# Kernel tuning notes

Measured on AMD Instinct MI355X. Metric: run time of the kernel, lower is better.

Reference implementation:

```python
import jax, jax.numpy as jnp
import numpy as np

B, T, D, H = 256, 512, 512, 512


def setup_inputs() -> dict:
    key = jax.random.key(0)
    k1, k2, k3, k4 = jax.random.split(key, 4)
    inputs = jax.random.normal(k1, (B, T, D), dtype=jnp.float32)
    lengths = jax.random.randint(k2, (B,), 0, T).astype(jnp.int32)
    # LSTM params. Flax nn.LSTMCell uses per-gate dense layers:
    #  input dense (with bias) and recurrent dense (no bias). Packing the
    #  four gates (i, f, g, o) into one matrix is mathematically identical.
    Wx = jax.random.normal(k3, (D, 4 * H), dtype=jnp.float32) * (1.0 / np.sqrt(D))
    Wh = jax.random.normal(k4, (H, 4 * H), dtype=jnp.float32) * (1.0 / np.sqrt(H))
    b = jnp.zeros((4 * H,), dtype=jnp.float32)
    return {"inputs": inputs, "lengths": lengths, "Wx": Wx, "Wh": Wh, "b": b}


def reference(inputs, lengths, Wx, Wh, b):
    batch = inputs.shape[0]
    hidden = Wh.shape[0]
    x_tbd = jnp.swapaxes(inputs, 0, 1)  # [T, B, D]

    def step(carry, x_t):
        c, h = carry
        # fused gate pre-activations: [B, 4H]
        z = x_t @ Wx + h @ Wh + b
        i, f, g, o = jnp.split(z, 4, axis=-1)
        i = jax.nn.sigmoid(i)
        f = jax.nn.sigmoid(f)
        g = jnp.tanh(g)
        o = jax.nn.sigmoid(o)
        c_new = f * c + i * g
        h_new = o * jnp.tanh(c_new)
        return (c_new, h_new), h_new

    c0 = jnp.zeros((batch, hidden), dtype=inputs.dtype)
    h0 = jnp.zeros((batch, hidden), dtype=inputs.dtype)
    _, hs = jax.lax.scan(step, (c0, h0), x_tbd)  # hs: [T, B, H]

    # select output at last valid timestep per example
    idx = jnp.maximum(0, lengths - 1)  # [B]
    return hs[idx, jnp.arange(batch), :]  # [B, H]
```

## Files before the change

### kernel.cpp

```cpp
#include <hip/hip_runtime.h>

#define Bb 256
#define Tt 512
#define Dd 512
#define Hh 512
#define KTOT 1024
#define FOURH 2048

typedef __attribute__((ext_vector_type(8))) short bf16x8;
typedef __attribute__((ext_vector_type(4))) float f32x4;

__device__ __forceinline__ unsigned short f2bf(float f) {
    union { float f; unsigned u; } x; x.f = f;
    unsigned u = x.u;
    unsigned r = u + 0x7FFFu + ((u >> 16) & 1u);
    return (unsigned short)(r >> 16);
}
__device__ __forceinline__ float bf2f(unsigned short s) {
    union { unsigned u; float f; } x; x.u = ((unsigned)s) << 16;
    return x.f;
}

__device__ __forceinline__ uint4 load16_sc01(const void* p) {
    uint4 v;
    asm volatile("global_load_dwordx4 %0, %1, off sc0 sc1" : "=v"(v) : "v"(p));
    return v;
}

__global__ void prep_w(const float* __restrict__ Wx, const float* __restrict__ Wh,
                       unsigned short* __restrict__ WT_hi, unsigned short* __restrict__ WT_lo) {
    __shared__ float tile[32][33];
    int n0 = (blockIdx.x & 63) * 32;
    int k0 = (blockIdx.x >> 6) * 32;
    int tx = threadIdx.x & 31;
    int ty = threadIdx.x >> 5;
    for (int q = 0; q < 4; ++q) {
        int k = k0 + ty + q * 8;
        int n = n0 + tx;
        float v = (k < Dd) ? Wx[(size_t)k * FOURH + n] : Wh[(size_t)(k - Dd) * FOURH + n];
        tile[ty + q * 8][tx] = v;
    }
    __syncthreads();
    for (int q = 0; q < 4; ++q) {
        int nl = ty + q * 8;
        int kl = tx;
        float v = tile[kl][nl];
        unsigned short hi = f2bf(v);
        unsigned short lo = f2bf(v - bf2f(hi));
        size_t o = (size_t)(n0 + nl) * KTOT + (size_t)(k0 + kl);
        WT_hi[o] = hi;
        WT_lo[o] = lo;
    }
}

__global__ void init_state3(char* __restrict__ ws, int persist) {
    long i = (long)blockIdx.x * blockDim.x + threadIdx.x;
    if (i < 98304) {
        *(uint4*)(ws + (8u << 20) + i * 16) = (uint4){0, 0, 0, 0};
    }
    if (persist && i < 512) {
        ((unsigned int*)(ws + (8u << 20) + (1536u << 10)))[i] = 0u;
    }
}

__global__ __launch_bounds__(512) void lstm_persist9(
    const float* __restrict__ X, const int* __restrict__ lengths,
    const unsigned short* __restrict__ WT_hi, const unsigned short* __restrict__ WT_lo,
    const float* __restrict__ bias,
    unsigned int* __restrict__ h_pack,
    unsigned int* __restrict__ ctrl,
    float* __restrict__ out)
{
    __shared__ unsigned short HLDS[32768];
    __shared__ unsigned short XLDS[32768];
    __shared__ float zbuf[8][32][17];

    const int bx = blockIdx.x;
    const int group = bx & 7;
    const int slot = bx >> 3;
    const int rt = slot & 7;
    const int cs = slot >> 3;
    const int r0 = rt * 32;
    const int j0h = group * 64 + cs * 16;
    const int tid = threadIdx.x;
    const int w8 = tid >> 6;
    const int lane = tid & 63;
    const int l15 = lane & 15;
    const int q4 = lane >> 4;
    const int klo = q4 * 8;
    const int gate = w8 & 3;
    const int khalf = w8 >> 2;

    const size_t HB = (size_t)Bb * Hh;

    const int colg = gate * 512 + j0h + l15;
    const size_t bbase = (size_t)colg * KTOT + (size_t)khalf * 512;
    const unsigned short* bhp = &WT_hi[bbase];
    const unsigned short* blp = &WT_lo[bbase];

    const int xr = tid >> 4;
    const int xk0 = (tid & 15) * 32;
    const float* xbase = &X[((size_t)(r0 + xr) * Tt) * Dd + xk0];

    const int er = tid >> 4;
    const int ej = tid & 15;
    const int row_g = r0 + er;
    const int col_h = j0h + ej;
    const size_t oidx = (size_t)row_g * Hh + col_h;
    int oT = lengths[row_g] - 1; if (oT < 0) oT = 0;
    const float b0 = bias[col_h], b1 = bias[512 + col_h],
                b2 = bias[1024 + col_h], b3 = bias[1536 + col_h];
    float creg = 0.f;

    unsigned int* myflag = &ctrl[rt * 32];

    for (int t = 0; t < Tt; ++t) {
        const int p_r = t & 1;
        const unsigned int* hp_r = h_pack + (size_t)p_r * HB;
        unsigned int* hp_w = h_pack + (size_t)(p_r ^ 1) * HB;

        uint4 hb[8];
#pragma unroll
        for (int it = 0; it < 4; ++it) {
            const int c = it * 512 + tid;
            const int row = c >> 6, k8 = c & 63;
            const unsigned int* p = hp_r + ((size_t)(r0 + row) * Hh + k8 * 8);
            hb[it * 2] = load16_sc01(p);
            hb[it * 2 + 1] = load16_sc01(p + 4);
        }

        {
            const float* xp = xbase + (size_t)t * Dd;
            float4 xv[8];
#pragma unroll
            for (int i = 0; i < 8; ++i) xv[i] = ((const float4*)xp)[i];
            const int ksx = tid & 15;
            const int mi = xr >> 4, lr = xr & 15;
#pragma unroll
            for (int c2 = 0; c2 < 4; ++c2) {
                float vv[8];
                *(float4*)&vv[0] = xv[2 * c2];
                *(float4*)&vv[4] = xv[2 * c2 + 1];
                bf16x8 hv8, lv8;
#pragma unroll
                for (int e = 0; e < 8; ++e) {
                    unsigned short hs = f2bf(vv[e]);
                    hv8[e] = (short)hs;
                    lv8[e] = (short)f2bf(vv[e] - bf2f(hs));
                }
                const int lnw = (c2 * 16 + lr) ^ (ksx & 7);
                *(bf16x8*)&XLDS[(((0 * 2 + mi) * 16 + ksx) * 64 + lnw) * 8] = hv8;
                *(bf16x8*)&XLDS[(((1 * 2 + mi) * 16 + ksx) * 64 + lnw) * 8] = lv8;
            }
        }

        asm volatile("s_waitcnt vmcnt(0)" ::: "memory");
        __builtin_amdgcn_sched_barrier(0);

#pragma unroll
        for (int it = 0; it < 4; ++it) {
            const int c = it * 512 + tid;
            const int row = c >> 6, k8 = c & 63;
            const int ksh = k8 >> 2, qq = k8 & 3;
            const int mi = row >> 4, lr = row & 15;
            const unsigned int u0 = hb[it * 2].x, u1 = hb[it * 2].y;
            const unsigned int u2 = hb[it * 2].z, u3 = hb[it * 2].w;
            const unsigned int u4 = hb[it * 2 + 1].x, u5 = hb[it * 2 + 1].y;
            const unsigned int u6 = hb[it * 2 + 1].z, u7 = hb[it * 2 + 1].w;
            uint4 hiw, low;
            hiw.x = (u0 >> 16) | (u1 & 0xffff0000u);
            hiw.y = (u2 >> 16) | (u3 & 0xffff0000u);
            hiw.z = (u4 >> 16) | (u5 & 0xffff0000u);
            hiw.w = (u6 >> 16) | (u7 & 0xffff0000u);
            low.x = (u0 & 0xffffu) | (u1 << 16);
            low.y = (u2 & 0xffffu) | (u3 << 16);
            low.z = (u4 & 0xffffu) | (u5 << 16);
            low.w = (u6 & 0xffffu) | (u7 << 16);
            const int lnw = (qq * 16 + lr) ^ (ksh & 7);
            *(uint4*)&HLDS[(((0 * 2 + mi) * 16 + ksh) * 64 + lnw) * 8] = hiw;
            *(uint4*)&HLDS[(((1 * 2 + mi) * 16 + ksh) * 64 + lnw) * 8] = low;
        }
        __syncthreads();

        const unsigned short* ALDS = khalf ? HLDS : XLDS;
        f32x4 acc[2][3];
#pragma unroll
        for (int mi = 0; mi < 2; ++mi)
#pragma unroll
            for (int s = 0; s < 3; ++s)
                acc[mi][s] = (f32x4){0.f, 0.f, 0.f, 0.f};

#pragma unroll
        for (int ks = 0; ks < 16; ++ks) {
            const int kk = ks * 32 + klo;
            const bf16x8 bh = *(const bf16x8*)&bhp[kk];
            const bf16x8 bl = *(const bf16x8*)&blp[kk];
            const int lnr = lane ^ (ks & 7);
#pragma unroll
            for (int mi = 0; mi < 2; ++mi) {
                const bf16x8 ah = *(const bf16x8*)&ALDS[(((0 * 2 + mi) * 16 + ks) * 64 + lnr) * 8];
                const bf16x8 al = *(const bf16x8*)&ALDS[(((1 * 2 + mi) * 16 + ks) * 64 + lnr) * 8];
                acc[mi][0] = __builtin_amdgcn_mfma_f32_16x16x32_bf16(ah, bh, acc[mi][0], 0, 0, 0);
                acc[mi][1] = __builtin_amdgcn_mfma_f32_16x16x32_bf16(ah, bl, acc[mi][1], 0, 0, 0);
                acc[mi][2] = __builtin_amdgcn_mfma_f32_16x16x32_bf16(al, bh, acc[mi][2], 0, 0, 0);
            }
        }

#pragma unroll
        for (int mi = 0; mi < 2; ++mi) {
            const f32x4 z = acc[mi][0] + acc[mi][1] + acc[mi][2];
#pragma unroll
            for (int r = 0; r < 4; ++r)
                zbuf[w8][mi * 16 + q4 * 4 + r][l15] = z[r];
        }
        __syncthreads();

        float zi = zbuf[0][er][ej] + zbuf[4][er][ej] + b0;
        float zf = zbuf[1][er][ej] + zbuf[5][er][ej] + b1;
        float zg = zbuf[2][er][ej] + zbuf[6][er][ej] + b2;
        float zo = zbuf[3][er][ej] + zbuf[7][er][ej] + b3;
        float ig = 1.f / (1.f + expf(-zi));
        float fg = 1.f / (1.f + expf(-zf));
        float gg = tanhf(zg);
        float og = 1.f / (1.f + expf(-zo));
        float cn = fg * creg + ig * gg;
        creg = cn;
        float hn = og * tanhf(cn);
        unsigned short hh = f2bf(hn);
        unsigned short hl = f2bf(hn - bf2f(hh));
        unsigned int up = ((unsigned int)hh << 16) | (unsigned int)hl;
        __hip_atomic_store(&hp_w[oidx], up, __ATOMIC_RELAXED, __HIP_MEMORY_SCOPE_SYSTEM);
        if (t == oT) out[oidx] = hn;

        if (t < Tt - 1) {
            asm volatile("s_waitcnt vmcnt(0)" ::: "memory");
            __syncthreads();
            if (tid == 0) {
                __hip_atomic_fetch_add(myflag, 1u, __ATOMIC_RELAXED, __HIP_MEMORY_SCOPE_SYSTEM);
                const unsigned int tgt = (unsigned int)(t + 1) * 32u;
                while (__hip_atomic_load(myflag, __ATOMIC_RELAXED, __HIP_MEMORY_SCOPE_SYSTEM) < tgt)
                    __builtin_amdgcn_s_sleep(2);
            }
            __syncthreads();
        }
    }
}

__global__ __launch_bounds__(512) void lstm_step4(
    const float* __restrict__ X, const int* __restrict__ lengths,
    const unsigned short* __restrict__ WT_hi, const unsigned short* __restrict__ WT_lo,
    const float* __restrict__ bias,
    float* __restrict__ c_st,
    const unsigned short* __restrict__ h_r_hi, const unsigned short* __restrict__ h_r_lo,
    unsigned short* __restrict__ h_w_hi, unsigned short* __restrict__ h_w_lo,
    float* __restrict__ out, int t)
{
    __shared__ float zbuf[8][16][17];

    const int bx = blockIdx.x;
    const int xcd = bx & 7;
    const int rem = bx >> 3;
    const int m0 = (rem & 15) * 16;
    const int col_group = xcd * 4 + (rem >> 4);
    const int hc0 = col_group * 16;
    const int tid = threadIdx.x;
    const int w8 = tid >> 6;
    const int lane = tid & 63;
    const int gate = w8 & 3;
    const int khalf = w8 >> 2;

    f32x4 ahh = (f32x4){0,0,0,0}, ahl = (f32x4){0,0,0,0}, alh = (f32x4){0,0,0,0};

    const int colk = gate * 512 + hc0 + (lane & 15);
    const size_t bbase = (size_t)colk * KTOT;
    const int klo = (lane >> 4) * 8;
    const int row = m0 + (lane & 15);

    if (khalf == 0) {
        const float* xrow = &X[((size_t)row * Tt + t) * Dd];
        const unsigned short* bhp = &WT_hi[bbase];
        const unsigned short* blp = &WT_lo[bbase];
#pragma unroll
        for (int ks = 0; ks < 16; ++ks) {
            const int kk = ks * 32 + klo;
            const float4 v0 = *(const float4*)&xrow[kk];
            const float4 v1 = *(const float4*)&xrow[kk + 4];
            float vv[8] = {v0.x, v0.y, v0.z, v0.w, v1.x, v1.y, v1.z, v1.w};
            bf16x8 ah, al;
#pragma unroll
            for (int e = 0; e < 8; ++e) {
                unsigned short hi = f2bf(vv[e]);
                ah[e] = (short)hi;
                al[e] = (short)f2bf(vv[e] - bf2f(hi));
            }
            const bf16x8 bh = *(const bf16x8*)&bhp[kk];
            const bf16x8 bl = *(const bf16x8*)&blp[kk];
            ahh = __builtin_amdgcn_mfma_f32_16x16x32_bf16(ah, bh, ahh, 0, 0, 0);
            ahl = __builtin_amdgcn_mfma_f32_16x16x32_bf16(ah, bl, ahl, 0, 0, 0);
            alh = __builtin_amdgcn_mfma_f32_16x16x32_bf16(al, bh, alh, 0, 0, 0);
        }
    } else {
        const unsigned short* hrh = &h_r_hi[(size_t)row * Hh];
        const unsigned short* hrl = &h_r_lo[(size_t)row * Hh];
        const unsigned short* bhp = &WT_hi[bbase + 512];
        const unsigned short* blp = &WT_lo[bbase + 512];
#pragma unroll
        for (int ks = 0; ks < 16; ++ks) {
            const int kk = ks * 32 + klo;
            const bf16x8 ah = *(const bf16x8*)&hrh[kk];
            const bf16x8 al = *(const bf16x8*)&hrl[kk];
            const bf16x8 bh = *(const bf16x8*)&bhp[kk];
            const bf16x8 bl = *(const bf16x8*)&blp[kk];
            ahh = __builtin_amdgcn_mfma_f32_16x16x32_bf16(ah, bh, ahh, 0, 0, 0);
            ahl = __builtin_amdgcn_mfma_f32_16x16x32_bf16(ah, bl, ahl, 0, 0, 0);
            alh = __builtin_amdgcn_mfma_f32_16x16x32_bf16(al, bh, alh, 0, 0, 0);
        }
    }

    const f32x4 z = ahh + ahl + alh;
#pragma unroll
    for (int r = 0; r < 4; ++r)
        zbuf[w8][(lane >> 4) * 4 + r][lane & 15] = z[r];
    __syncthreads();

    if (tid < 256) {
        const int r = tid >> 4;
        const int j = tid & 15;
        const int row_g = m0 + r;
        const int col_g = hc0 + j;
        float zi = zbuf[0][r][j] + zbuf[4][r][j] + bias[col_g];
        float zf = zbuf[1][r][j] + zbuf[5][r][j] + bias[512 + col_g];
        float zg = zbuf[2][r][j] + zbuf[6][r][j] + bias[1024 + col_g];
        float zo = zbuf[3][r][j] + zbuf[7][r][j] + bias[1536 + col_g];
        float ig = 1.f / (1.f + expf(-zi));
        float fg = 1.f / (1.f + expf(-zf));
        float gg = tanhf(zg);
        float og = 1.f / (1.f + expf(-zo));
        const size_t idx = (size_t)row_g * Hh + col_g;
        float cn = fg * c_st[idx] + ig * gg;
        float hn = og * tanhf(cn);
        c_st[idx] = cn;
        unsigned short hh = f2bf(hn);
        h_w_hi[idx] = hh;
        h_w_lo[idx] = f2bf(hn - bf2f(hh));
        int len = lengths[row_g];
        int oidx = len - 1; if (oidx < 0) oidx = 0;
        if (t == oidx) out[idx] = hn;
    }
}

extern "C" void kernel_launch(void* const* d_in, const int* in_sizes, int n_in,
                              void* d_out, int out_size, void* d_ws, size_t ws_size,
                              hipStream_t stream) {
    const float* X = (const float*)d_in[0];
    const int* lengths = (const int*)d_in[1];
    const float* Wx = (const float*)d_in[2];
    const float* Wh = (const float*)d_in[3];
    const float* bias = (const float*)d_in[4];
    float* out = (float*)d_out;

    char* ws = (char*)d_ws;
    unsigned short* WT_hi = (unsigned short*)ws;
    unsigned short* WT_lo = (unsigned short*)(ws + (4u << 20));
    unsigned int* h_pack = (unsigned int*)(ws + (8u << 20));
    unsigned int* ctrl = (unsigned int*)(ws + (8u << 20) + (1536u << 10));
    float* c_st = (float*)(ws + (8u << 20));
    unsigned short* h_base = (unsigned short*)(ws + (8u << 20) + (512u << 10));
    const size_t HB = (size_t)Bb * Hh;
    unsigned short* h_hi0 = h_base;
    unsigned short* h_lo0 = h_base + HB;
    unsigned short* h_hi1 = h_base + 2 * HB;
    unsigned short* h_lo1 = h_base + 3 * HB;

    const size_t NEED_PERSIST = (8u << 20) + (1536u << 10) + 4096u;
    const int can_persist = (ws_size >= NEED_PERSIST) ? 1 : 0;

    hipLaunchKernelGGL(prep_w, dim3(2048), dim3(256), 0, stream, Wx, Wh, WT_hi, WT_lo);
    hipLaunchKernelGGL(init_state3, dim3(512), dim3(256), 0, stream, ws, can_persist);

    hipError_t err = hipErrorUnknown;
    if (can_persist) {
        void* args[] = { (void*)&X, (void*)&lengths, (void*)&WT_hi, (void*)&WT_lo,
                         (void*)&bias, (void*)&h_pack, (void*)&ctrl, (void*)&out };
        err = hipLaunchCooperativeKernel((const void*)lstm_persist9,
                                         dim3(256), dim3(512), args, 0, stream);
    }
    if (err != hipSuccess) {
        for (int t = 0; t < Tt; ++t) {
            const bool even = (t & 1) == 0;
            hipLaunchKernelGGL(lstm_step4, dim3(512), dim3(512), 0, stream,
                               X, lengths, WT_hi, WT_lo, bias, c_st,
                               even ? h_hi0 : h_hi1, even ? h_lo0 : h_lo1,
                               even ? h_hi1 : h_hi0, even ? h_lo1 : h_lo0,
                               out, t);
        }
    }
}
```

Measured before the change: 7.107 ms.

## Exchange hidden state as int16 fixed-point and retile persistent LSTM blocks

```diff
diff --git a/kernel.cpp b/kernel.cpp
--- a/kernel.cpp
+++ b/kernel.cpp
@@ -25,6 +25,16 @@
     uint4 v;
     asm volatile("global_load_dwordx4 %0, %1, off sc0 sc1" : "=v"(v) : "v"(p));
     return v;
+}
+
+__device__ __forceinline__ void i16_to_bf(int v, unsigned short& bh, unsigned short& bl) {
+    int vh = v >> 8;
+    int vl = v & 255;
+    union { float f; unsigned u; } a, b;
+    a.f = (float)vh * 0.0078125f;
+    b.f = (float)vl * 3.0517578125e-05f;
+    bh = (unsigned short)(a.u >> 16);
+    bl = (unsigned short)(b.u >> 16);
 }
 
 __global__ void prep_w(const float* __restrict__ Wx, const float* __restrict__ Wh,
@@ -63,25 +73,23 @@
     }
 }
 
-__global__ __launch_bounds__(512) void lstm_persist9(
+__global__ __launch_bounds__(512) void lstm_persist10(
     const float* __restrict__ X, const int* __restrict__ lengths,
     const unsigned short* __restrict__ WT_hi, const unsigned short* __restrict__ WT_lo,
     const float* __restrict__ bias,
-    unsigned int* __restrict__ h_pack,
+    short* __restrict__ h_i16,
     unsigned int* __restrict__ ctrl,
     float* __restrict__ out)
 {
-    __shared__ unsigned short HLDS[32768];
-    __shared__ unsigned short XLDS[32768];
-    __shared__ float zbuf[8][32][17];
+    __shared__ unsigned short ALDS[32768];
+    __shared__ float zbuf[8][16][17];
 
     const int bx = blockIdx.x;
-    const int group = bx & 7;
-    const int slot = bx >> 3;
-    const int rt = slot & 7;
-    const int cs = slot >> 3;
-    const int r0 = rt * 32;
-    const int j0h = group * 64 + cs * 16;
+    const int g = bx & 7;
+    const int cb = g * 2 + ((bx >> 3) & 1);
+    const int rt = bx >> 4;
+    const int r0 = rt * 16;
+    const int ch0 = cb * 32;
     const int tid = threadIdx.x;
     const int w8 = tid >> 6;
     const int lane = tid & 63;
@@ -89,55 +97,52 @@
     const int q4 = lane >> 4;
     const int klo = q4 * 8;
     const int gate = w8 & 3;
-    const int khalf = w8 >> 2;
+    const int chalf = w8 >> 2;
 
     const size_t HB = (size_t)Bb * Hh;
 
-    const int colg = gate * 512 + j0h + l15;
-    const size_t bbase = (size_t)colg * KTOT + (size_t)khalf * 512;
+    const int colg = gate * 512 + ch0 + chalf * 16 + l15;
+    const size_t bbase = (size_t)colg * KTOT;
     const unsigned short* bhp = &WT_hi[bbase];
     const unsigned short* blp = &WT_lo[bbase];
 
-    const int xr = tid >> 4;
-    const int xk0 = (tid & 15) * 32;
-    const float* xbase = &X[((size_t)(r0 + xr) * Tt) * Dd + xk0];
-
-    const int er = tid >> 4;
-    const int ej = tid & 15;
+    const int xr = tid >> 5;
+    const int xc = tid & 31;
+    const float* xbase = &X[((size_t)(r0 + xr) * Tt) * Dd + xc * 16];
+
+    const int hr = tid >> 5;
+    const int j = tid & 31;
+
+    const int er = tid >> 5;
+    const int ej = tid & 31;
     const int row_g = r0 + er;
-    const int col_h = j0h + ej;
+    const int col_h = ch0 + ej;
     const size_t oidx = (size_t)row_g * Hh + col_h;
     int oT = lengths[row_g] - 1; if (oT < 0) oT = 0;
     const float b0 = bias[col_h], b1 = bias[512 + col_h],
                 b2 = bias[1024 + col_h], b3 = bias[1536 + col_h];
+    const int ech = ej >> 4;
+    const int ecj = ej & 15;
     float creg = 0.f;
 
     unsigned int* myflag = &ctrl[rt * 32];
 
     for (int t = 0; t < Tt; ++t) {
         const int p_r = t & 1;
-        const unsigned int* hp_r = h_pack + (size_t)p_r * HB;
-        unsigned int* hp_w = h_pack + (size_t)(p_r ^ 1) * HB;
-
-        uint4 hb[8];
-#pragma unroll
-        for (int it = 0; it < 4; ++it) {
-            const int c = it * 512 + tid;
-            const int row = c >> 6, k8 = c & 63;
-            const unsigned int* p = hp_r + ((size_t)(r0 + row) * Hh + k8 * 8);
-            hb[it * 2] = load16_sc01(p);
-            hb[it * 2 + 1] = load16_sc01(p + 4);
-        }
+        const short* hp_r = h_i16 + (size_t)p_r * HB;
+        short* hp_w = h_i16 + (size_t)(p_r ^ 1) * HB;
+
+        const short* hsrc = hp_r + (size_t)(r0 + hr) * Hh + j * 16;
+        uint4 ha = load16_sc01(hsrc);
+        uint4 hb2 = load16_sc01(hsrc + 8);
 
         {
             const float* xp = xbase + (size_t)t * Dd;
-            float4 xv[8];
-#pragma unroll
-            for (int i = 0; i < 8; ++i) xv[i] = ((const float4*)xp)[i];
-            const int ksx = tid & 15;
-            const int mi = xr >> 4, lr = xr & 15;
-#pragma unroll
-            for (int c2 = 0; c2 < 4; ++c2) {
+            float4 xv[4];
+#pragma unroll
+            for (int i = 0; i < 4; ++i) xv[i] = ((const float4*)xp)[i];
+#pragma unroll
+            for (int c2 = 0; c2 < 2; ++c2) {
                 float vv[8];
                 *(float4*)&vv[0] = xv[2 * c2];
                 *(float4*)&vv[4] = xv[2 * c2 + 1];
@@ -148,9 +153,12 @@
                     hv8[e] = (short)hs;
                     lv8[e] = (short)f2bf(vv[e] - bf2f(hs));
                 }
-                const int lnw = (c2 * 16 + lr) ^ (ksx & 7);
-                *(bf16x8*)&XLDS[(((0 * 2 + mi) * 16 + ksx) * 64 + lnw) * 8] = hv8;
-                *(bf16x8*)&XLDS[(((1 * 2 + mi) * 16 + ksx) * 64 + lnw) * 8] = lv8;
+                const int k = xc * 16 + c2 * 8;
+                const int ks = k >> 5;
+                const int qq = (k >> 3) & 3;
+                const int slot = (qq * 16 + xr) ^ (ks & 7);
+                *(bf16x8*)&ALDS[((0 * 32 + ks) * 64 + slot) * 8] = hv8;
+                *(bf16x8*)&ALDS[((1 * 32 + ks) * 64 + slot) * 8] = lv8;
             }
         }
 
@@ -158,67 +166,52 @@
         __builtin_amdgcn_sched_barrier(0);
 
 #pragma unroll
-        for (int it = 0; it < 4; ++it) {
-            const int c = it * 512 + tid;
-            const int row = c >> 6, k8 = c & 63;
-            const int ksh = k8 >> 2, qq = k8 & 3;
-            const int mi = row >> 4, lr = row & 15;
-            const unsigned int u0 = hb[it * 2].x, u1 = hb[it * 2].y;
-            const unsigned int u2 = hb[it * 2].z, u3 = hb[it * 2].w;
-            const unsigned int u4 = hb[it * 2 + 1].x, u5 = hb[it * 2 + 1].y;
-            const unsigned int u6 = hb[it * 2 + 1].z, u7 = hb[it * 2 + 1].w;
-            uint4 hiw, low;
-            hiw.x = (u0 >> 16) | (u1 & 0xffff0000u);
-            hiw.y = (u2 >> 16) | (u3 & 0xffff0000u);
-            hiw.z = (u4 >> 16) | (u5 & 0xffff0000u);
-            hiw.w = (u6 >> 16) | (u7 & 0xffff0000u);
-            low.x = (u0 & 0xffffu) | (u1 << 16);
-            low.y = (u2 & 0xffffu) | (u3 << 16);
-            low.z = (u4 & 0xffffu) | (u5 << 16);
-            low.w = (u6 & 0xffffu) | (u7 << 16);
-            const int lnw = (qq * 16 + lr) ^ (ksh & 7);
-            *(uint4*)&HLDS[(((0 * 2 + mi) * 16 + ksh) * 64 + lnw) * 8] = hiw;
-            *(uint4*)&HLDS[(((1 * 2 + mi) * 16 + ksh) * 64 + lnw) * 8] = low;
+        for (int b = 0; b < 2; ++b) {
+            const uint4 q = b ? hb2 : ha;
+            const unsigned qs[4] = {q.x, q.y, q.z, q.w};
+            bf16x8 ahv, alv;
+#pragma unroll
+            for (int e = 0; e < 4; ++e) {
+                const unsigned u = qs[e];
+                unsigned short bh0, bl0, bh1, bl1;
+                i16_to_bf((int)(short)(u & 0xffffu), bh0, bl0);
+                i16_to_bf((int)(short)(u >> 16), bh1, bl1);
+                ahv[2 * e] = (short)bh0; alv[2 * e] = (short)bl0;
+                ahv[2 * e + 1] = (short)bh1; alv[2 * e + 1] = (short)bl1;
+            }
+            const int blk = 2 * j + b;
+            const int ks = 16 + (blk >> 2);
+            const int qq = blk & 3;
+            const int slot = (qq * 16 + hr) ^ (ks & 7);
+            *(bf16x8*)&ALDS[((0 * 32 + ks) * 64 + slot) * 8] = ahv;
+            *(bf16x8*)&ALDS[((1 * 32 + ks) * 64 + slot) * 8] = alv;
         }
         __syncthreads();
 
-        const unsigned short* ALDS = khalf ? HLDS : XLDS;
-        f32x4 acc[2][3];
-#pragma unroll
-        for (int mi = 0; mi < 2; ++mi)
-#pragma unroll
-            for (int s = 0; s < 3; ++s)
-                acc[mi][s] = (f32x4){0.f, 0.f, 0.f, 0.f};
-
-#pragma unroll
-        for (int ks = 0; ks < 16; ++ks) {
+        f32x4 acc0 = (f32x4){0,0,0,0}, acc1 = (f32x4){0,0,0,0}, acc2 = (f32x4){0,0,0,0};
+#pragma unroll
+        for (int ks = 0; ks < 32; ++ks) {
             const int kk = ks * 32 + klo;
             const bf16x8 bh = *(const bf16x8*)&bhp[kk];
             const bf16x8 bl = *(const bf16x8*)&blp[kk];
-            const int lnr = lane ^ (ks & 7);
-#pragma unroll
-            for (int mi = 0; mi < 2; ++mi) {
-                const bf16x8 ah = *(const bf16x8*)&ALDS[(((0 * 2 + mi) * 16 + ks) * 64 + lnr) * 8];
-                const bf16x8 al = *(const bf16x8*)&ALDS[(((1 * 2 + mi) * 16 + ks) * 64 + lnr) * 8];
-                acc[mi][0] = __builtin_amdgcn_mfma_f32_16x16x32_bf16(ah, bh, acc[mi][0], 0, 0, 0);
-                acc[mi][1] = __builtin_amdgcn_mfma_f32_16x16x32_bf16(ah, bl, acc[mi][1], 0, 0, 0);
-                acc[mi][2] = __builtin_amdgcn_mfma_f32_16x16x32_bf16(al, bh, acc[mi][2], 0, 0, 0);
-            }
-        }
-
-#pragma unroll
-        for (int mi = 0; mi < 2; ++mi) {
-            const f32x4 z = acc[mi][0] + acc[mi][1] + acc[mi][2];
-#pragma unroll
-            for (int r = 0; r < 4; ++r)
-                zbuf[w8][mi * 16 + q4 * 4 + r][l15] = z[r];
-        }
+            const int slotr = lane ^ (ks & 7);
+            const bf16x8 ah = *(const bf16x8*)&ALDS[((0 * 32 + ks) * 64 + slotr) * 8];
+            const bf16x8 al = *(const bf16x8*)&ALDS[((1 * 32 + ks) * 64 + slotr) * 8];
+            acc0 = __builtin_amdgcn_mfma_f32_16x16x32_bf16(ah, bh, acc0, 0, 0, 0);
+            acc1 = __builtin_amdgcn_mfma_f32_16x16x32_bf16(ah, bl, acc1, 0, 0, 0);
+            acc2 = __builtin_amdgcn_mfma_f32_16x16x32_bf16(al, bh, acc2, 0, 0, 0);
+        }
+
+        const f32x4 z = acc0 + acc1 + acc2;
+#pragma unroll
+        for (int r = 0; r < 4; ++r)
+            zbuf[w8][q4 * 4 + r][l15] = z[r];
         __syncthreads();
 
-        float zi = zbuf[0][er][ej] + zbuf[4][er][ej] + b0;
-        float zf = zbuf[1][er][ej] + zbuf[5][er][ej] + b1;
-        float zg = zbuf[2][er][ej] + zbuf[6][er][ej] + b2;
-        float zo = zbuf[3][er][ej] + zbuf[7][er][ej] + b3;
+        float zi = zbuf[ech * 4 + 0][er][ecj] + b0;
+        float zf = zbuf[ech * 4 + 1][er][ecj] + b1;
+        float zg = zbuf[ech * 4 + 2][er][ecj] + b2;
+        float zo = zbuf[ech * 4 + 3][er][ecj] + b3;
         float ig = 1.f / (1.f + expf(-zi));
         float fg = 1.f / (1.f + expf(-zf));
         float gg = tanhf(zg);
@@ -226,10 +219,9 @@
         float cn = fg * creg + ig * gg;
         creg = cn;
         float hn = og * tanhf(cn);
-        unsigned short hh = f2bf(hn);
-        unsigned short hl = f2bf(hn - bf2f(hh));
-        unsigned int up = ((unsigned int)hh << 16) | (unsigned int)hl;
-        __hip_atomic_store(&hp_w[oidx], up, __ATOMIC_RELAXED, __HIP_MEMORY_SCOPE_SYSTEM);
+        int vi = __float2int_rn(hn * 32768.f);
+        vi = vi > 32767 ? 32767 : (vi < -32767 ? -32767 : vi);
+        __hip_atomic_store(&hp_w[oidx], (short)vi, __ATOMIC_RELAXED, __HIP_MEMORY_SCOPE_SYSTEM);
         if (t == oT) out[oidx] = hn;
 
         if (t < Tt - 1) {
@@ -237,7 +229,7 @@
             __syncthreads();
             if (tid == 0) {
                 __hip_atomic_fetch_add(myflag, 1u, __ATOMIC_RELAXED, __HIP_MEMORY_SCOPE_SYSTEM);
-                const unsigned int tgt = (unsigned int)(t + 1) * 32u;
+                const unsigned int tgt = (unsigned int)(t + 1) * 16u;
                 while (__hip_atomic_load(myflag, __ATOMIC_RELAXED, __HIP_MEMORY_SCOPE_SYSTEM) < tgt)
                     __builtin_amdgcn_s_sleep(2);
             }
@@ -362,7 +354,7 @@
     char* ws = (char*)d_ws;
     unsigned short* WT_hi = (unsigned short*)ws;
     unsigned short* WT_lo = (unsigned short*)(ws + (4u << 20));
-    unsigned int* h_pack = (unsigned int*)(ws + (8u << 20));
+    short* h_i16 = (short*)(ws + (8u << 20));
     unsigned int* ctrl = (unsigned int*)(ws + (8u << 20) + (1536u << 10));
     float* c_st = (float*)(ws + (8u << 20));
     unsigned short* h_base = (unsigned short*)(ws + (8u << 20) + (512u << 10));
@@ -381,8 +373,8 @@
     hipError_t err = hipErrorUnknown;
     if (can_persist) {
         void* args[] = { (void*)&X, (void*)&lengths, (void*)&WT_hi, (void*)&WT_lo,
-                         (void*)&bias, (void*)&h_pack, (void*)&ctrl, (void*)&out };
-        err = hipLaunchCooperativeKernel((const void*)lstm_persist9,
+                         (void*)&bias, (void*)&h_i16, (void*)&ctrl, (void*)&out };
+        err = hipLaunchCooperativeKernel((const void*)lstm_persist10,
                                          dim3(256), dim3(512), args, 0, stream);
     }
     if (err != hipSuccess) {
```

Result: slower. 9.021 ms (+26.9%).
